# Kernel tuning notes

Measured on AMD Instinct MI355X. Metric: run time of the kernel, lower is better.

The kernel has to match this reference:

```python
import jax, jax.numpy as jnp
import numpy as np

D = 512
H = 8
HD = D // H

def setup_inputs() -> dict:
    key = jax.random.key(0)
    ks = jax.random.split(key, 16)
    B, L = 8, 384
    s = 1.0 / np.sqrt(D)
    inp = {
        "hidden_states": jax.random.normal(ks[0], (B, L, D), jnp.float32),
        "position_embeddings": jax.random.normal(ks[1], (L, L, D), jnp.float32),
        "attention_mask": jnp.ones((B, L), jnp.int32),
        "ln_g": jnp.ones((D,), jnp.float32),
        "ln_b": jnp.zeros((D,), jnp.float32),
        "Wq": jax.random.normal(ks[2], (D, D), jnp.float32) * s,
        "bq": jnp.zeros((D,), jnp.float32),
        "Wk": jax.random.normal(ks[3], (D, D), jnp.float32) * s,
        "bk": jnp.zeros((D,), jnp.float32),
        "Wv": jax.random.normal(ks[4], (D, D), jnp.float32) * s,
        "bv": jnp.zeros((D,), jnp.float32),
        "Wpos": jax.random.normal(ks[5], (D, D), jnp.float32) * s,
        "pos_bias_u": jax.random.normal(ks[6], (H, HD), jnp.float32) * 0.02,
        "pos_bias_v": jax.random.normal(ks[7], (H, HD), jnp.float32) * 0.02,
        "Wo": jax.random.normal(ks[8], (D, D), jnp.float32) * s,
        "bo": jnp.zeros((D,), jnp.float32),
    }
    return inp

def _layernorm(x, g, b, eps=1e-5):
    mu = jnp.mean(x, axis=-1, keepdims=True)
    var = jnp.var(x, axis=-1, keepdims=True)
    return (x - mu) * jax.lax.rsqrt(var + eps) * g + b

def reference(hidden_states, position_embeddings, attention_mask,
              ln_g, ln_b, Wq, bq, Wk, bk, Wv, bv, Wpos,
              pos_bias_u, pos_bias_v, Wo, bo):
    B, L, _ = hidden_states.shape
    x = _layernorm(hidden_states, ln_g, ln_b)
    # projections -> (B, L, H, HD)
    q = (x @ Wq.T + bq).reshape(B, L, H, HD)
    k = (x @ Wk.T + bk).reshape(B, L, H, HD)
    v = (x @ Wv.T + bv).reshape(B, L, H, HD)
    # relative position projection -> (H, L, L, HD); pos[h, i, j, d]
    pos = (position_embeddings @ Wpos.T).reshape(L, L, H, HD)
    pos = jnp.transpose(pos, (2, 0, 1, 3))
    q_u = q + pos_bias_u  # (B, L, H, HD)
    q_v = q + pos_bias_v
    # content score: ac[b,h,i,j] = sum_d q_u[b,i,h,d] * k[b,j,h,d]
    scores_ac = jnp.einsum('bihd,bjhd->bhij', q_u, k)
    # positional score (torch broadcast semantics): bd[b,h,i,j] = sum_d q_v[b,j,h,d] * pos[h,i,j,d]
    scores_bd = jnp.einsum('bjhd,hijd->bhij', q_v, pos)
    scores = (scores_ac + scores_bd) / np.sqrt(HD)
    mask = attention_mask[:, None, None, :]  # (B,1,1,L)
    scores = jnp.where(mask == 0, jnp.finfo(scores.dtype).min, scores)
    probs = jax.nn.softmax(scores, axis=-1)
    ctx = jnp.einsum('bhij,bjhd->bihd', probs, v).reshape(B, L, D)
    return ctx @ Wo.T + bo
```

## Files before the change

### kernel.cpp

```cpp
#include <hip/hip_runtime.h>
#include <hip/hip_bf16.h>

#define DEV __device__ __forceinline__

typedef short short8 __attribute__((ext_vector_type(8)));
typedef float f32x4 __attribute__((ext_vector_type(4)));
typedef unsigned short ushort4v __attribute__((ext_vector_type(4)));
typedef unsigned short u16;

DEV u16 f2b(float x){ __hip_bfloat16 h = __float2bfloat16(x); u16 u; __builtin_memcpy(&u, &h, 2); return u; }

DEV int swz(int row, int cb){ return row*128 + (cb ^ ((row & 7) << 4)); }
DEV int swz768(int row, int byte_in_row){ return row*768 + (byte_in_row ^ ((row & 7) << 4)); }

DEV short8 ldfrag(const u16* s, int row, int kbf){
  return *(const short8*)((const char*)s + swz(row, kbf*2));
}
DEV void st16(u16* s, int row, int cb, short8 v){
  *(short8*)((char*)s + swz(row, cb)) = v;
}
DEV f32x4 MFMA(short8 a, short8 b, f32x4 c){
  return __builtin_amdgcn_mfma_f32_16x16x32_bf16(a, b, c, 0, 0, 0);
}

template<int R>
DEV void stage_bf16(u16* lds, const u16* g, size_t rstride, int tid){
  #pragma unroll
  for (int c = tid; c < R*8; c += 256){
    int row = c >> 3, k = c & 7;
    short8 v = *(const short8*)(g + (size_t)row*rstride + k*8);
    st16(lds, row, k*16, v);
  }
}

template<int R>
DEV void stage_f32(u16* lds, const float* g, size_t rstride, int tid){
  #pragma unroll
  for (int c = tid; c < R*8; c += 256){
    int row = c >> 3, k = c & 7;
    const float* p = g + (size_t)row*rstride + k*8;
    f32x4 f0 = *(const f32x4*)p;
    f32x4 f1 = *(const f32x4*)(p + 4);
    short8 v;
    #pragma unroll
    for (int t = 0; t < 4; ++t){ v[t] = (short)f2b(f0[t]); v[t+4] = (short)f2b(f1[t]); }
    st16(lds, row, k*16, v);
  }
}

template<int MI, int NI>
DEV void mma_step(const u16* As, int ar0, const u16* Bs, int br0, f32x4 (&acc)[MI][NI], int lane){
  int r = lane & 15, kb = (lane >> 4) * 8;
  #pragma unroll
  for (int kk = 0; kk < 64; kk += 32){
    short8 a[MI], b[NI];
    #pragma unroll
    for (int mi = 0; mi < MI; ++mi) a[mi] = ldfrag(As, ar0 + mi*16 + r, kk + kb);
    #pragma unroll
    for (int ni = 0; ni < NI; ++ni) b[ni] = ldfrag(Bs, br0 + ni*16 + r, kk + kb);
    #pragma unroll
    for (int mi = 0; mi < MI; ++mi)
      #pragma unroll
      for (int ni = 0; ni < NI; ++ni)
        acc[mi][ni] = MFMA(a[mi], b[ni], acc[mi][ni]);
  }
}

__global__ __launch_bounds__(256) void k_qkv(const float* __restrict__ hs,
    const float* __restrict__ lg, const float* __restrict__ lb,
    const float* __restrict__ Wq, const float* __restrict__ Wk, const float* __restrict__ Wv,
    const float* __restrict__ bq, const float* __restrict__ bk, const float* __restrict__ bv,
    const float* __restrict__ pbu, const float* __restrict__ pbv,
    u16* __restrict__ qu, u16* __restrict__ qv, u16* __restrict__ kkb, u16* __restrict__ vt){
  __shared__ __align__(16) u16 As[128*64];
  __shared__ __align__(16) u16 Bs[128*64];
  __shared__ float ps[2][128], ps2[2][128], mus[128], rss[128];
  __shared__ float gs[512], bss[512];
  int tid = threadIdx.x, lane = tid & 63, wid = tid >> 6;
  int t0 = blockIdx.x * 128, n0 = blockIdx.y * 128, z = blockIdx.z;
  const float* W    = (z==0) ? Wq : (z==1) ? Wk : Wv;
  const float* bias = (z==0) ? bq : (z==1) ? bk : bv;

  {
    int row = tid & 127, hf = tid >> 7;
    const f32x4* p = (const f32x4*)(hs + (size_t)(t0+row)*512 + hf*256);
    float s = 0.f, s2 = 0.f;
    #pragma unroll 8
    for (int c = 0; c < 64; ++c){
      f32x4 v = p[c];
      #pragma unroll
      for (int t = 0; t < 4; ++t){ s += v[t]; s2 += v[t]*v[t]; }
    }
    ps[hf][row] = s; ps2[hf][row] = s2;
  }
  gs[tid] = lg[tid]; gs[tid+256] = lg[tid+256];
  bss[tid] = lb[tid]; bss[tid+256] = lb[tid+256];
  __syncthreads();
  if (tid < 128){
    float S = ps[0][tid] + ps[1][tid], S2 = ps2[0][tid] + ps2[1][tid];
    float mu = S * (1.0f/512.0f);
    float var = S2 * (1.0f/512.0f) - mu*mu;
    mus[tid] = mu; rss[tid] = rsqrtf(var + 1e-5f);
  }

  f32x4 acc[4][4] = {};
  for (int k0 = 0; k0 < 512; k0 += 64){
    __syncthreads();
    #pragma unroll
    for (int c = tid; c < 1024; c += 256){
      int rw = c >> 3, k = c & 7;
      const float* pp = hs + (size_t)(t0+rw)*512 + k0 + k*8;
      f32x4 f0 = *(const f32x4*)pp;
      f32x4 f1 = *(const f32x4*)(pp + 4);
      float mu = mus[rw], rs = rss[rw];
      short8 v;
      #pragma unroll
      for (int t = 0; t < 4; ++t){
        int e = k0 + k*8 + t;
        v[t]   = (short)f2b((f0[t]-mu)*rs*gs[e]   + bss[e]);
        v[t+4] = (short)f2b((f1[t]-mu)*rs*gs[e+4] + bss[e+4]);
      }
      st16(As, rw, k*16, v);
    }
    stage_f32<128>(Bs, W + (size_t)n0*512 + k0, 512, tid);
    __syncthreads();
    mma_step<4,4>(As, (wid>>1)*64, Bs, (wid&1)*64, acc, lane);
  }
  int r = lane & 15, half = lane >> 4;
  #pragma unroll
  for (int mi = 0; mi < 4; ++mi)
  #pragma unroll
  for (int ni = 0; ni < 4; ++ni){
    int n = n0 + (wid&1)*64 + ni*16 + r;
    int h = n >> 6, d = n & 63;
    int m0 = t0 + (wid>>1)*64 + mi*16 + half*4;
    #pragma unroll
    for (int q = 0; q < 4; ++q){
      int t = m0 + q, b = t / 384, i = t - b*384;
      float v = acc[mi][ni][q] + bias[n];
      if (z == 0){
        qu[((size_t)(b*8+h)*384 + i)*64 + d] = f2b(v + pbu[n]);
        qv[((size_t)h*3072 + t)*64 + d]      = f2b(v + pbv[n]);
      } else if (z == 1){
        kkb[((size_t)(b*8+h)*384 + i)*64 + d] = f2b(v);
      } else {
        vt[((size_t)(b*8+h)*64 + d)*384 + i] = f2b(v);
      }
    }
  }
}

__global__ __launch_bounds__(256) void k_qw(const u16* __restrict__ qv, const float* __restrict__ Wpos,
                                            u16* __restrict__ qW){
  __shared__ __align__(16) u16 As[128*64];
  __shared__ __align__(16) u16 Bs[128*64];
  int tid = threadIdx.x, lane = tid & 63, wid = tid >> 6;
  int t0 = blockIdx.x * 128, e0 = blockIdx.y * 128, h = blockIdx.z;
  f32x4 acc[4][4] = {};
  stage_bf16<128>(As, qv + ((size_t)h*3072 + t0)*64, 64, tid);
  #pragma unroll
  for (int c = tid; c < 1024; c += 256){
    int e = c >> 3, k = c & 7;
    short8 v;
    #pragma unroll
    for (int t = 0; t < 8; ++t)
      v[t] = (short)f2b(Wpos[(size_t)(h*64 + k*8 + t)*512 + e0 + e]);
    st16(Bs, e, k*16, v);
  }
  __syncthreads();
  mma_step<4,4>(As, (wid>>1)*64, Bs, (wid&1)*64, acc, lane);
  int r = lane & 15, half = lane >> 4;
  #pragma unroll
  for (int mi = 0; mi < 4; ++mi)
  #pragma unroll
  for (int ni = 0; ni < 4; ++ni){
    int e = e0 + (wid&1)*64 + ni*16 + r;
    int m0 = t0 + (wid>>1)*64 + mi*16 + half*4;
    #pragma unroll
    for (int q = 0; q < 4; ++q){
      int t = m0 + q, b = t / 384, j = t - b*384;
      int bh = b*8 + h;
      qW[((size_t)bh*384 + j)*512 + e] = f2b(acc[mi][ni][q]);
    }
  }
}

__global__ __launch_bounds__(256, 3) void k_bd(const u16* __restrict__ qW, const float* __restrict__ P,
                                               float* __restrict__ Sbd){
  __shared__ __align__(16) u16 As[64*256];
  int tid = threadIdx.x, lane = tid & 63, wid = tid >> 6;
  int r = lane & 15, half = lane >> 4;
  int ib = blockIdx.x * 192, j = blockIdx.y;

  const float* Bp[3];
  #pragma unroll
  for (int ni = 0; ni < 3; ++ni){
    int i = ib + wid*48 + ni*16 + r;
    Bp[ni] = P + ((size_t)i*384 + j)*512 + half*8;
  }
  const u16* Ag = qW + (size_t)j*512;

  f32x4 acc[4][3] = {};
  #pragma unroll
  for (int kh = 0; kh < 2; ++kh){
    if (kh) __syncthreads();
    #pragma unroll
    for (int s = 0; s < 8; ++s){
      int c = tid + s*256;
      int bh = c >> 5, c16 = c & 31;
      short8 v = *(const short8*)(Ag + (size_t)bh*(384*512) + kh*256 + c16*8);
      *(short8*)((char*)As + bh*512 + ((c16*16) ^ ((bh & 7) << 4))) = v;
    }
    __syncthreads();
    #pragma unroll
    for (int k32 = 0; k32 < 8; ++k32){
      int e0 = kh*256 + k32*32;
      short8 bfr[3];
      #pragma unroll
      for (int ni = 0; ni < 3; ++ni){
        f32x4 f0 = *(const f32x4*)(Bp[ni] + e0);
        f32x4 f1 = *(const f32x4*)(Bp[ni] + e0 + 4);
        #pragma unroll
        for (int t = 0; t < 4; ++t){ bfr[ni][t] = (short)f2b(f0[t]); bfr[ni][t+4] = (short)f2b(f1[t]); }
      }
      #pragma unroll
      for (int mi = 0; mi < 4; ++mi){
        int row = mi*16 + r;
        short8 afr = *(const short8*)((const char*)As + row*512 + ((k32*64 + half*16) ^ ((row & 7) << 4)));
        #pragma unroll
        for (int ni = 0; ni < 3; ++ni)
          acc[mi][ni] = MFMA(afr, bfr[ni], acc[mi][ni]);
      }
    }
  }
  #pragma unroll
  for (int mi = 0; mi < 4; ++mi)
  #pragma unroll
  for (int ni = 0; ni < 3; ++ni){
    int i = ib + wid*48 + ni*16 + r;
    #pragma unroll
    for (int q = 0; q < 4; ++q){
      int bh = mi*16 + half*4 + q;
      Sbd[((size_t)j*64 + bh)*384 + i] = acc[mi][ni][q];
    }
  }
}

__global__ __launch_bounds__(256) void k_fin(const u16* __restrict__ qu, const u16* __restrict__ kkb,
                                             const u16* __restrict__ vt, const float* __restrict__ Sbd,
                                             const int* __restrict__ mask, u16* __restrict__ ctx){
  __shared__ __align__(16) u16 Ks[384*64];
  __shared__ __align__(16) u16 Qs[96*64];
  __shared__ __align__(16) u16 Vs[64*384];
  __shared__ __align__(16) u16 Ps[32*384];
  __shared__ float smbuf[2][4][2][16];
  int tid = threadIdx.x, lane = tid & 63, wid = tid >> 6;
  int r = lane & 15, half = lane >> 4;
  int i0 = blockIdx.x * 96, bh = blockIdx.y, b = bh >> 3, h = bh & 7;

  stage_bf16<384>(Ks, kkb + (size_t)bh*384*64, 64, tid);
  stage_bf16<96>(Qs, qu + ((size_t)bh*384 + i0)*64, 64, tid);
  #pragma unroll
  for (int c = tid; c < 3072; c += 256){
    int d = c / 48, jc = c - d*48;
    short8 v = *(const short8*)(vt + ((size_t)bh*64 + d)*384 + jc*8);
    *(short8*)((char*)Vs + swz768(d, jc*16)) = v;
  }
  __syncthreads();

  for (int sub = 0; sub < 3; ++sub){
    int i0s = i0 + sub*32;
    f32x4 acc[6][2] = {};
    mma_step<6,2>(Ks, wid*96, Qs, sub*32, acc, lane);

    int jw = wid*96 + half*4;
    #pragma unroll
    for (int mi = 0; mi < 6; ++mi){
      #pragma unroll
      for (int q = 0; q < 4; ++q){
        int j = jw + mi*16 + q;
        bool dead = (mask[b*384 + j] == 0);
        const float* srow = Sbd + ((size_t)j*64 + bh)*384 + i0s;
        #pragma unroll
        for (int ni = 0; ni < 2; ++ni){
          float v = (acc[mi][ni][q] + srow[ni*16 + r]) * 0.125f;
          acc[mi][ni][q] = dead ? -3.402823466e38f : v;
        }
      }
    }

    float mx[2];
    #pragma unroll
    for (int ni = 0; ni < 2; ++ni){
      float m = -3.402823466e38f;
      #pragma unroll
      for (int mi = 0; mi < 6; ++mi){
        f32x4 a = acc[mi][ni];
        m = fmaxf(m, fmaxf(fmaxf(a[0],a[1]), fmaxf(a[2],a[3])));
      }
      m = fmaxf(m, __shfl_xor(m, 16));
      m = fmaxf(m, __shfl_xor(m, 32));
      mx[ni] = m;
    }
    if (lane < 16){ smbuf[0][wid][0][r] = mx[0]; smbuf[0][wid][1][r] = mx[1]; }
    __syncthreads();
    #pragma unroll
    for (int ni = 0; ni < 2; ++ni)
      mx[ni] = fmaxf(fmaxf(smbuf[0][0][ni][r], smbuf[0][1][ni][r]),
                     fmaxf(smbuf[0][2][ni][r], smbuf[0][3][ni][r]));

    float sum[2] = {0.f, 0.f};
    #pragma unroll
    for (int ni = 0; ni < 2; ++ni){
      #pragma unroll
      for (int mi = 0; mi < 6; ++mi)
        #pragma unroll
        for (int q = 0; q < 4; ++q){
          float e = __expf(acc[mi][ni][q] - mx[ni]);
          acc[mi][ni][q] = e; sum[ni] += e;
        }
      sum[ni] += __shfl_xor(sum[ni], 16);
      sum[ni] += __shfl_xor(sum[ni], 32);
    }
    if (lane < 16){ smbuf[1][wid][0][r] = sum[0]; smbuf[1][wid][1][r] = sum[1]; }
    __syncthreads();
    float inv[2];
    #pragma unroll
    for (int ni = 0; ni < 2; ++ni)
      inv[ni] = 1.0f / (smbuf[1][0][ni][r] + smbuf[1][1][ni][r] + smbuf[1][2][ni][r] + smbuf[1][3][ni][r]);

    #pragma unroll
    for (int mi = 0; mi < 6; ++mi){
      int jb = jw + mi*16;
      #pragma unroll
      for (int ni = 0; ni < 2; ++ni){
        int i = ni*16 + r;
        ushort4v pk;
        #pragma unroll
        for (int q = 0; q < 4; ++q) pk[q] = f2b(acc[mi][ni][q] * inv[ni]);
        *(ushort4v*)((char*)Ps + swz768(i, jb*2)) = pk;
      }
    }
    __syncthreads();

    f32x4 acc2[2] = {};
    #pragma unroll
    for (int ks = 0; ks < 384; ks += 32){
      int j0 = ks + half*8;
      short8 bfr = *(const short8*)((const char*)Vs + swz768(wid*16 + r, j0*2));
      #pragma unroll
      for (int mi = 0; mi < 2; ++mi){
        short8 afr = *(const short8*)((const char*)Ps + swz768(mi*16 + r, j0*2));
        acc2[mi] = MFMA(afr, bfr, acc2[mi]);
      }
    }
    #pragma unroll
    for (int mi = 0; mi < 2; ++mi)
      #pragma unroll
      for (int q = 0; q < 4; ++q){
        int i = i0s + mi*16 + half*4 + q;
        int d = wid*16 + r;
        ctx[((size_t)(b*384 + i))*512 + h*64 + d] = f2b(acc2[mi][q]);
      }
  }
}

__global__ __launch_bounds__(256) void k_out(const u16* __restrict__ ctx, const float* __restrict__ Wo,
                                             const float* __restrict__ bo, float* __restrict__ out){
  __shared__ __align__(16) u16 As[64*64];
  __shared__ __align__(16) u16 Bs[64*64];
  int tid = threadIdx.x, lane = tid & 63, wid = tid >> 6;
  int t0 = blockIdx.x * 64, n0 = blockIdx.y * 64;
  f32x4 acc[2][2] = {};
  for (int k0 = 0; k0 < 512; k0 += 64){
    stage_bf16<64>(As, ctx + (size_t)t0*512 + k0, 512, tid);
    stage_f32<64>(Bs, Wo + (size_t)n0*512 + k0, 512, tid);
    __syncthreads();
    mma_step<2,2>(As, (wid>>1)*32, Bs, (wid&1)*32, acc, lane);
    __syncthreads();
  }
  int r = lane & 15, half = lane >> 4;
  #pragma unroll
  for (int mi = 0; mi < 2; ++mi)
  #pragma unroll
  for (int ni = 0; ni < 2; ++ni){
    int n = n0 + (wid&1)*32 + ni*16 + r;
    int m0 = t0 + (wid>>1)*32 + mi*16 + half*4;
    #pragma unroll
    for (int q = 0; q < 4; ++q){
      int t = m0 + q;
      out[(size_t)t*512 + n] = acc[mi][ni][q] + bo[n];
    }
  }
}

extern "C" void kernel_launch(void* const* d_in, const int* in_sizes, int n_in,
                              void* d_out, int out_size, void* d_ws, size_t ws_size,
                              hipStream_t stream) {
  const float* hs   = (const float*)d_in[0];
  const float* P    = (const float*)d_in[1];
  const int*   mask = (const int*)d_in[2];
  const float* ln_g = (const float*)d_in[3];
  const float* ln_b = (const float*)d_in[4];
  const float* Wq   = (const float*)d_in[5];
  const float* bq   = (const float*)d_in[6];
  const float* Wk   = (const float*)d_in[7];
  const float* bk   = (const float*)d_in[8];
  const float* Wv   = (const float*)d_in[9];
  const float* bv   = (const float*)d_in[10];
  const float* Wpos = (const float*)d_in[11];
  const float* pbu  = (const float*)d_in[12];
  const float* pbv  = (const float*)d_in[13];
  const float* Wo   = (const float*)d_in[14];
  const float* bo   = (const float*)d_in[15];
  float* out = (float*)d_out;

  char* w = (char*)d_ws;
  u16* qu  = (u16*)w;   w += (size_t)3072*512*2;
  u16* qv  = (u16*)w;   w += (size_t)3072*512*2;
  u16* kkb = (u16*)w;   w += (size_t)3072*512*2;
  u16* vt  = (u16*)w;   w += (size_t)3072*512*2;
  u16* ctx = (u16*)w;   w += (size_t)3072*512*2;
  u16* qW  = (u16*)w;   w += (size_t)64*384*512*2;
  float* Sbd = (float*)w; w += (size_t)64*384*384*4;

  k_qkv<<<dim3(24,4,3), 256, 0, stream>>>(hs, ln_g, ln_b, Wq, Wk, Wv, bq, bk, bv, pbu, pbv, qu, qv, kkb, vt);
  k_qw <<<dim3(24,4,8), 256, 0, stream>>>(qv, Wpos, qW);
  k_bd <<<dim3(2,384), 256, 0, stream>>>(qW, P, Sbd);
  k_fin<<<dim3(4,64), 256, 0, stream>>>(qu, kkb, vt, Sbd, mask, ctx);
  k_out<<<dim3(48,8), 256, 0, stream>>>(ctx, Wo, bo, out);
}
```

Baseline: 180.1 us.

## Pre-transpose Wpos to bf16 and double k_fin threads to 512

A new kernel k_wpt transposes and converts Wpos to bf16 once per call, so k_qw can stage its B operand with plain 16-byte bf16 loads instead of strided fp32 gathers. k_fin now runs 512 threads (8 waves), so each wave covers 48 key rows instead of 96 and the PV product is split across 8 waves. The cross-wave softmax reductions are widened to 8 waves. The aim is more latency hiding and less per-wave work in the attention kernel, at the cost of an extra launch and more waves contending for the same LDS.

```diff
diff --git a/kernel.cpp b/kernel.cpp
--- a/kernel.cpp
+++ b/kernel.cpp
@@ -150,7 +150,29 @@
   }
 }
 
-__global__ __launch_bounds__(256) void k_qw(const u16* __restrict__ qv, const float* __restrict__ Wpos,
+__global__ __launch_bounds__(256) void k_wpt(const float* __restrict__ Wpos, u16* __restrict__ Wpt){
+  __shared__ float ws[64][65];
+  int tid = threadIdx.x;
+  int e0 = (blockIdx.x & 7) * 64, h = blockIdx.x >> 3;
+  #pragma unroll
+  for (int p = tid; p < 64*16; p += 256){
+    int d = p >> 4, q = p & 15;
+    f32x4 v = *(const f32x4*)(Wpos + (size_t)(h*64 + d)*512 + e0 + q*4);
+    #pragma unroll
+    for (int t = 0; t < 4; ++t) ws[d][q*4+t] = v[t];
+  }
+  __syncthreads();
+  #pragma unroll
+  for (int c = tid; c < 64*8; c += 256){
+    int e = c >> 3, dc = c & 7;
+    short8 v;
+    #pragma unroll
+    for (int t = 0; t < 8; ++t) v[t] = (short)f2b(ws[dc*8+t][e]);
+    *(short8*)(Wpt + ((size_t)h*512 + e0 + e)*64 + dc*8) = v;
+  }
+}
+
+__global__ __launch_bounds__(256) void k_qw(const u16* __restrict__ qv, const u16* __restrict__ Wpt,
                                             u16* __restrict__ qW){
   __shared__ __align__(16) u16 As[128*64];
   __shared__ __align__(16) u16 Bs[128*64];
@@ -158,15 +180,7 @@
   int t0 = blockIdx.x * 128, e0 = blockIdx.y * 128, h = blockIdx.z;
   f32x4 acc[4][4] = {};
   stage_bf16<128>(As, qv + ((size_t)h*3072 + t0)*64, 64, tid);
-  #pragma unroll
-  for (int c = tid; c < 1024; c += 256){
-    int e = c >> 3, k = c & 7;
-    short8 v;
-    #pragma unroll
-    for (int t = 0; t < 8; ++t)
-      v[t] = (short)f2b(Wpos[(size_t)(h*64 + k*8 + t)*512 + e0 + e]);
-    st16(Bs, e, k*16, v);
-  }
+  stage_bf16<128>(Bs, Wpt + ((size_t)h*512 + e0)*64, 64, tid);
   __syncthreads();
   mma_step<4,4>(As, (wid>>1)*64, Bs, (wid&1)*64, acc, lane);
   int r = lane & 15, half = lane >> 4;
@@ -246,22 +260,32 @@
   }
 }
 
-__global__ __launch_bounds__(256) void k_fin(const u16* __restrict__ qu, const u16* __restrict__ kkb,
+__global__ __launch_bounds__(512) void k_fin(const u16* __restrict__ qu, const u16* __restrict__ kkb,
                                              const u16* __restrict__ vt, const float* __restrict__ Sbd,
                                              const int* __restrict__ mask, u16* __restrict__ ctx){
   __shared__ __align__(16) u16 Ks[384*64];
   __shared__ __align__(16) u16 Qs[96*64];
   __shared__ __align__(16) u16 Vs[64*384];
   __shared__ __align__(16) u16 Ps[32*384];
-  __shared__ float smbuf[2][4][2][16];
+  __shared__ float smbuf[2][8][2][16];
   int tid = threadIdx.x, lane = tid & 63, wid = tid >> 6;
   int r = lane & 15, half = lane >> 4;
   int i0 = blockIdx.x * 96, bh = blockIdx.y, b = bh >> 3, h = bh & 7;
 
-  stage_bf16<384>(Ks, kkb + (size_t)bh*384*64, 64, tid);
-  stage_bf16<96>(Qs, qu + ((size_t)bh*384 + i0)*64, 64, tid);
-  #pragma unroll
-  for (int c = tid; c < 3072; c += 256){
+  #pragma unroll
+  for (int c = tid; c < 3072; c += 512){
+    int row = c >> 3, k = c & 7;
+    short8 v = *(const short8*)(kkb + ((size_t)bh*384 + row)*64 + k*8);
+    st16(Ks, row, k*16, v);
+  }
+  #pragma unroll
+  for (int c = tid; c < 768; c += 512){
+    int row = c >> 3, k = c & 7;
+    short8 v = *(const short8*)(qu + ((size_t)bh*384 + i0 + row)*64 + k*8);
+    st16(Qs, row, k*16, v);
+  }
+  #pragma unroll
+  for (int c = tid; c < 3072; c += 512){
     int d = c / 48, jc = c - d*48;
     short8 v = *(const short8*)(vt + ((size_t)bh*64 + d)*384 + jc*8);
     *(short8*)((char*)Vs + swz768(d, jc*16)) = v;
@@ -270,12 +294,12 @@
 
   for (int sub = 0; sub < 3; ++sub){
     int i0s = i0 + sub*32;
-    f32x4 acc[6][2] = {};
-    mma_step<6,2>(Ks, wid*96, Qs, sub*32, acc, lane);
-
-    int jw = wid*96 + half*4;
-    #pragma unroll
-    for (int mi = 0; mi < 6; ++mi){
+    f32x4 acc[3][2] = {};
+    mma_step<3,2>(Ks, wid*48, Qs, sub*32, acc, lane);
+
+    int jw = wid*48 + half*4;
+    #pragma unroll
+    for (int mi = 0; mi < 3; ++mi){
       #pragma unroll
       for (int q = 0; q < 4; ++q){
         int j = jw + mi*16 + q;
@@ -294,7 +318,7 @@
     for (int ni = 0; ni < 2; ++ni){
       float m = -3.402823466e38f;
       #pragma unroll
-      for (int mi = 0; mi < 6; ++mi){
+      for (int mi = 0; mi < 3; ++mi){
         f32x4 a = acc[mi][ni];
         m = fmaxf(m, fmaxf(fmaxf(a[0],a[1]), fmaxf(a[2],a[3])));
       }
@@ -305,15 +329,18 @@
     if (lane < 16){ smbuf[0][wid][0][r] = mx[0]; smbuf[0][wid][1][r] = mx[1]; }
     __syncthreads();
     #pragma unroll
-    for (int ni = 0; ni < 2; ++ni)
-      mx[ni] = fmaxf(fmaxf(smbuf[0][0][ni][r], smbuf[0][1][ni][r]),
-                     fmaxf(smbuf[0][2][ni][r], smbuf[0][3][ni][r]));
+    for (int ni = 0; ni < 2; ++ni){
+      float m = smbuf[0][0][ni][r];
+      #pragma unroll
+      for (int w = 1; w < 8; ++w) m = fmaxf(m, smbuf[0][w][ni][r]);
+      mx[ni] = m;
+    }
 
     float sum[2] = {0.f, 0.f};
     #pragma unroll
     for (int ni = 0; ni < 2; ++ni){
       #pragma unroll
-      for (int mi = 0; mi < 6; ++mi)
+      for (int mi = 0; mi < 3; ++mi)
         #pragma unroll
         for (int q = 0; q < 4; ++q){
           float e = __expf(acc[mi][ni][q] - mx[ni]);
@@ -326,11 +353,15 @@
     __syncthreads();
     float inv[2];
     #pragma unroll
-    for (int ni = 0; ni < 2; ++ni)
-      inv[ni] = 1.0f / (smbuf[1][0][ni][r] + smbuf[1][1][ni][r] + smbuf[1][2][ni][r] + smbuf[1][3][ni][r]);
-
-    #pragma unroll
-    for (int mi = 0; mi < 6; ++mi){
+    for (int ni = 0; ni < 2; ++ni){
+      float s = smbuf[1][0][ni][r];
+      #pragma unroll
+      for (int w = 1; w < 8; ++w) s += smbuf[1][w][ni][r];
+      inv[ni] = 1.0f / s;
+    }
+
+    #pragma unroll
+    for (int mi = 0; mi < 3; ++mi){
       int jb = jw + mi*16;
       #pragma unroll
       for (int ni = 0; ni < 2; ++ni){
@@ -343,25 +374,21 @@
     }
     __syncthreads();
 
-    f32x4 acc2[2] = {};
+    int mih = wid >> 2, dq = wid & 3;
+    f32x4 acc2 = {};
     #pragma unroll
     for (int ks = 0; ks < 384; ks += 32){
       int j0 = ks + half*8;
-      short8 bfr = *(const short8*)((const char*)Vs + swz768(wid*16 + r, j0*2));
-      #pragma unroll
-      for (int mi = 0; mi < 2; ++mi){
-        short8 afr = *(const short8*)((const char*)Ps + swz768(mi*16 + r, j0*2));
-        acc2[mi] = MFMA(afr, bfr, acc2[mi]);
-      }
-    }
-    #pragma unroll
-    for (int mi = 0; mi < 2; ++mi)
-      #pragma unroll
-      for (int q = 0; q < 4; ++q){
-        int i = i0s + mi*16 + half*4 + q;
-        int d = wid*16 + r;
-        ctx[((size_t)(b*384 + i))*512 + h*64 + d] = f2b(acc2[mi][q]);
-      }
+      short8 bfr = *(const short8*)((const char*)Vs + swz768(dq*16 + r, j0*2));
+      short8 afr = *(const short8*)((const char*)Ps + swz768(mih*16 + r, j0*2));
+      acc2 = MFMA(afr, bfr, acc2);
+    }
+    #pragma unroll
+    for (int q = 0; q < 4; ++q){
+      int i = i0s + mih*16 + half*4 + q;
+      int d = dq*16 + r;
+      ctx[((size_t)(b*384 + i))*512 + h*64 + d] = f2b(acc2[q]);
+    }
   }
 }
 
@@ -420,13 +447,15 @@
   u16* qv  = (u16*)w;   w += (size_t)3072*512*2;
   u16* kkb = (u16*)w;   w += (size_t)3072*512*2;
   u16* vt  = (u16*)w;   w += (size_t)3072*512*2;
+  u16* Wpt = (u16*)w;   w += (size_t)8*512*64*2;
   u16* ctx = (u16*)w;   w += (size_t)3072*512*2;
   u16* qW  = (u16*)w;   w += (size_t)64*384*512*2;
   float* Sbd = (float*)w; w += (size_t)64*384*384*4;
 
+  k_wpt<<<64, 256, 0, stream>>>(Wpos, Wpt);
   k_qkv<<<dim3(24,4,3), 256, 0, stream>>>(hs, ln_g, ln_b, Wq, Wk, Wv, bq, bk, bv, pbu, pbv, qu, qv, kkb, vt);
-  k_qw <<<dim3(24,4,8), 256, 0, stream>>>(qv, Wpos, qW);
+  k_qw <<<dim3(24,4,8), 256, 0, stream>>>(qv, Wpt, qW);
   k_bd <<<dim3(2,384), 256, 0, stream>>>(qW, P, Sbd);
-  k_fin<<<dim3(4,64), 256, 0, stream>>>(qu, kkb, vt, Sbd, mask, ctx);
+  k_fin<<<dim3(4,64), 512, 0, stream>>>(qu, kkb, vt, Sbd, mask, ctx);
   k_out<<<dim3(48,8), 256, 0, stream>>>(ctx, Wo, bo, out);
 }
```

New measurement: 175.9 us. 1.02x faster.
